# Kernel optimization log

Measured on AMD Instinct MI355X. Metric: run time of the kernel, lower is better.

Reference implementation:

```python
import jax, jax.numpy as jnp
import numpy as np

N = 50000      # node_size
D = 256        # node_F == rel_F (ent_F)
R = 1000       # rel_size
E = 300000     # triple_size == n_edges
DEPTH = 2
KSEL = E // 2  # rows rewritten by W_orth transform
NPROXY = 128


def l2n(x):
    # tf.nn.l2_normalize with eps=1e-12
    return x * jax.lax.rsqrt(jnp.maximum(jnp.sum(x * x, axis=-1, keepdims=True), 1e-12))


def setup_inputs() -> dict:
    key = jax.random.key(0)
    ks = jax.random.split(key, 12)
    features = jax.random.normal(ks[0], (N, D), jnp.float32)
    rel_emb = jax.random.normal(ks[1], (R, D), jnp.float32)
    p = jax.random.normal(ks[2], (N, 1), jnp.float32)            # dynamic_node_kernel
    w_keys = jax.random.normal(ks[3], (DEPTH, D, D), jnp.float32) / np.float32(np.sqrt(D))
    attn_kernels = jax.random.normal(ks[4], (DEPTH, D, 1), jnp.float32) * 0.1
    proxy = jax.random.normal(ks[5], (NPROXY, D * (DEPTH + 1)), jnp.float32) * 0.05
    gate_kernel = jax.random.normal(ks[6], (D * (DEPTH + 1), D * (DEPTH + 1)), jnp.float32) / np.float32(np.sqrt(D * (DEPTH + 1)))
    adj_row = jnp.sort(jax.random.randint(ks[7], (E,), 0, N))    # destination (segment) ids, sorted
    adj_col = jax.random.randint(ks[8], (E,), 0, N)              # neighbor ids
    rel_ids = jax.random.randint(ks[9], (E,), 0, R)              # relation id per triple/edge
    rel_vals = jax.random.uniform(ks[10], (E,), jnp.float32)     # sparse_val per triple
    new_indices = jax.random.randint(ks[11], (KSEL,), 0, E)      # rows updated by w_key
    return dict(features=features, rel_emb=rel_emb, p=p, w_keys=w_keys,
                attn_kernels=attn_kernels, proxy=proxy, gate_kernel=gate_kernel,
                rel_vals=rel_vals, adj_row=adj_row, adj_col=adj_col,
                rel_ids=rel_ids, new_indices=new_indices)


def reference(features, rel_emb, p, w_keys, attn_kernels, proxy, gate_kernel,
              rel_vals, adj_row, adj_col, rel_ids, new_indices):
    tanh_p = jnp.tanh(p)                                   # [N,1]
    feats = features * tanh_p                              # use_p scaling (activation=None -> identity)
    outputs = [feats]
    for l in range(DEPTH):
        # sparse (triple,rel) x rel_emb : one relation per triple -> gather + scale
        rels_sum = rel_vals[:, None] * rel_emb[rel_ids]    # [E,D]
        rels_sum = l2n(rels_sum)
        # W_orth: transform a subset of rows by w_key, scatter back
        src = rels_sum[new_indices] @ w_keys[l]            # [KSEL,D]
        rels_sum = rels_sum.at[new_indices].set(src)
        neighs = feats[adj_col]                            # [E,D] gather
        rels_sum = rels_sum * tanh_p[adj_col]              # use_p on neighbors
        # Householder-style reflection of neighbor features
        neighs = neighs - 2.0 * jnp.sum(neighs * rels_sum, axis=1, keepdims=True) * rels_sum
        # per-edge attention logits, softmax over incoming edges of each row node
        att = (rels_sum @ attn_kernels[l])[:, 0]           # [E]
        m = jax.ops.segment_max(att, adj_row, num_segments=N)      # [N]
        att = jnp.exp(att - m[adj_row])
        s = jax.ops.segment_sum(att, adj_row, num_segments=N)      # [N]
        att = att / s[adj_row]
        # weighted scatter-aggregate
        feats = jax.ops.segment_sum(neighs * att[:, None], adj_row, num_segments=N)  # [N,D]
        feats = feats * tanh_p
        outputs.append(feats)
    out = jnp.concatenate(outputs, axis=-1)                # [N, D*(DEPTH+1)]
    proxy_att = jax.nn.softmax(l2n(out) @ l2n(proxy).T, axis=-1)   # [N,128]
    proxy_feature = out - proxy_att @ proxy
    gate = jax.nn.sigmoid(proxy_feature @ gate_kernel)
    out = gate * out + (1.0 - gate) * proxy_feature
    return (out, p)
```

## Files before the change

kernel.cpp:

```cpp
#include <hip/hip_runtime.h>
#include <math.h>

#define D 256
#define DCAT 768
#define NPX 128
#define QSTR 896
#define CSTR 136

typedef __attribute__((ext_vector_type(8))) short bf16x8;
typedef __attribute__((ext_vector_type(4))) float f32x4;

__device__ __forceinline__ short cvt_bf16(float f){
  union { float f; unsigned u; } v; v.f = f;
  unsigned r = v.u + 0x7FFF + ((v.u >> 16) & 1);
  return (short)(r >> 16);
}
__device__ __forceinline__ float bf2f(short s){
  union { float f; unsigned u; } v; v.u = ((unsigned)(unsigned short)s) << 16;
  return v.f;
}

__device__ __forceinline__ float waveSum(float v){
#pragma unroll
  for(int o=32;o>=1;o>>=1) v += __shfl_xor(v,o,64);
  return v;
}
__device__ __forceinline__ float waveMax(float v){
#pragma unroll
  for(int o=32;o>=1;o>>=1) v = fmaxf(v,__shfl_xor(v,o,64));
  return v;
}

__global__ void k_setup(const float* __restrict__ rel_emb, const float* __restrict__ attn,
                        const float* __restrict__ w_keys, const float* __restrict__ proxy,
                        const float* __restrict__ gatek, const float* __restrict__ p,
                        const float* __restrict__ features,
                        const int* __restrict__ adj_row, const int* __restrict__ new_idx,
                        float* __restrict__ ss_rel, float* __restrict__ att_n,
                        float* __restrict__ att_t, short* __restrict__ reb,
                        short* __restrict__ rwb, short* __restrict__ pn,
                        short* __restrict__ BG, short* __restrict__ Bt2,
                        float* __restrict__ tp, int* __restrict__ rs,
                        unsigned char* __restrict__ flag, float* __restrict__ pout,
                        short* __restrict__ Q, float* __restrict__ ssn,
                        int R_, int n, int e, int ksel, int nprep){
  __shared__ float tile[32][33];
  __shared__ float tile2[32][33];
  __shared__ float sm[4];
  const int b = blockIdx.x, tid = threadIdx.x;
  const int lane = tid & 63, wv = tid >> 6;
  const int B2 = 3*R_+128, B3 = B2+576, B4 = B3+96, B5 = B4+96;
  const int B6 = B5+nprep;

  if(b < R_){
    int r = b, d = tid;
    float v = rel_emb[(size_t)r*D+d];
    reb[(size_t)r*D+d] = cvt_bf16(v);
    float s = waveSum(v*v);
    if(lane==0) sm[wv]=s;
    __syncthreads();
    if(tid==0) ss_rel[r]=sm[0]+sm[1]+sm[2]+sm[3];
    __syncthreads();
    for(int l=0;l<2;l++){
      float dd = waveSum(v*attn[l*D+d]);
      if(lane==0) sm[wv]=dd;
      __syncthreads();
      if(tid==0) att_n[(size_t)l*R_+r]=sm[0]+sm[1]+sm[2]+sm[3];
      __syncthreads();
    }
  } else if(b < 3*R_){
    int l = (b-R_) / R_, r = (b-R_) % R_, d = tid;
    const float* W = w_keys + (size_t)l*D*D;
    const float* ak = attn + (size_t)l*D;
    const float* row = rel_emb + (size_t)r*D;
    float acc=0.f;
#pragma unroll 4
    for(int k=0;k<D;k++) acc = fmaf(row[k], W[(size_t)k*D+d], acc);
    rwb[(size_t)l*R_*D + (size_t)r*D + d]=cvt_bf16(acc);
    float dd = waveSum(acc*ak[d]);
    if(lane==0) sm[wv]=dd;
    __syncthreads();
    if(tid==0) att_t[(size_t)l*R_+r]=sm[0]+sm[1]+sm[2]+sm[3];
  } else if(b < B2){
    int j = b - 3*R_;
    float v0 = proxy[(size_t)j*DCAT + tid];
    float v1 = proxy[(size_t)j*DCAT + 256 + tid];
    float v2 = proxy[(size_t)j*DCAT + 512 + tid];
    float ssum = waveSum(v0*v0 + v1*v1 + v2*v2);
    if(lane==0) sm[wv]=ssum;
    __syncthreads();
    float scale = rsqrtf(fmaxf(sm[0]+sm[1]+sm[2]+sm[3],1e-12f));
    pn[(size_t)j*DCAT + tid]       = cvt_bf16(v0*scale);
    pn[(size_t)j*DCAT + 256 + tid] = cvt_bf16(v1*scale);
    pn[(size_t)j*DCAT + 512 + tid] = cvt_bf16(v2*scale);
  } else if(b < B4){
    const float* in; short* out; int R, C, ldo, t;
    if(b < B3){ t = b-B2; in=gatek; out=BG;  R=DCAT; C=DCAT; ldo=QSTR; }
    else      { t = b-B3; in=proxy; out=Bt2; R=NPX;  C=DCAT; ldo=NPX;  }
    int bx = (t%24)*32, by = (t/24)*32;
    int tx = tid & 31, ty = tid >> 5;
    for(int i=ty;i<32;i+=8){
      int rr = by+i, cc = bx+tx;
      if(rr<R && cc<C) tile[i][tx] = in[(size_t)rr*C + cc];
    }
    __syncthreads();
    for(int i=ty;i<32;i+=8){
      int cc = bx+i, rr = by+tx;
      if(cc<C && rr<R) out[(size_t)cc*ldo + rr] = cvt_bf16(tile[tx][i]);
    }
  } else if(b < B5){
    int t = b - B4;
    int it = t / 24, jt = t % 24;
    int i0 = it*32, j0 = jt*32;
    int tx = tid & 31, ty = tid >> 5;
    float acc4[4] = {0.f,0.f,0.f,0.f};
    for(int k0=0;k0<DCAT;k0+=32){
      for(int rr=ty;rr<32;rr+=8){
        tile[rr][tx]  = proxy[(size_t)(i0+rr)*DCAT + k0+tx];
        tile2[rr][tx] = gatek[(size_t)(k0+rr)*DCAT + j0+tx];
      }
      __syncthreads();
#pragma unroll 8
      for(int kk=0;kk<32;kk++){
        float bv = tile2[kk][tx];
        acc4[0] = fmaf(tile[ty][kk],    bv, acc4[0]);
        acc4[1] = fmaf(tile[ty+8][kk],  bv, acc4[1]);
        acc4[2] = fmaf(tile[ty+16][kk], bv, acc4[2]);
        acc4[3] = fmaf(tile[ty+24][kk], bv, acc4[3]);
      }
      __syncthreads();
    }
#pragma unroll
    for(int k=0;k<4;k++)
      BG[(size_t)(j0+tx)*QSTR + DCAT + i0 + ty + 8*k] = cvt_bf16(-acc4[k]);
  } else if(b < B6){
    int t = b - B5;
    int i = t*256 + tid;
    if(i<n){ float pv = p[i]; tp[i]=tanhf(pv); pout[i]=pv; }
    if(i<=n){
      int lo=0, hi=e;
      while(lo<hi){ int mid=(lo+hi)>>1; if(adj_row[mid]<i) lo=mid+1; else hi=mid; }
      rs[i]=lo;
    }
    if(i<ksel) flag[new_idx[i]] = 1;
  } else {
    int row = b - B6;
    if(row < n){
      float t0 = tanhf(p[row]);
      float v = features[(size_t)row*D + tid] * t0;
      Q[(size_t)row*QSTR + tid] = cvt_bf16(v);
      float s = waveSum(v*v);
      if(lane==0) sm[wv]=s;
      __syncthreads();
      if(tid==0) ssn[row] = sm[0]+sm[1]+sm[2]+sm[3];
    }
  }
}

__global__ void k_agg(const int* __restrict__ rs, const int* __restrict__ adj_col,
                      const int* __restrict__ rel_ids, const float* __restrict__ rel_vals,
                      const unsigned char* __restrict__ flag, const float* __restrict__ tp,
                      const float* __restrict__ ss_rel, const float* __restrict__ att_n,
                      const float* __restrict__ att_t, const short* __restrict__ reb,
                      const short* __restrict__ rwb, short* __restrict__ Q,
                      float* __restrict__ ssn, int n, int layer){
  int wid = threadIdx.x>>6, lane = threadIdx.x&63;
  int node = blockIdx.x*4 + wid;
  if(node>=n) return;
  int s = rs[node], e = rs[node+1];
  float accq[16];
#pragma unroll
  for(int k=0;k<16;k++) accq[k]=0.f;

  auto logit = [&](int i)->float{
    int rid = rel_ids[i]; float rv = rel_vals[i];
    float a = 0.f;
    if(rv>0.f){
      float t = tp[adj_col[i]];
      float sc = rv*rsqrtf(fmaxf(rv*rv*ss_rel[rid],1e-12f));
      a = t*sc*(flag[i]? att_t[rid] : att_n[rid]);
    }
    return a;
  };

  if(e > s){
    float aF = 0.f, mxl = -INFINITY;
    {
      int i = s + lane;
      if(i < e){
        aF = logit(i);
        mxl = aF;
        for(i += 64; i < e; i += 64) mxl = fmaxf(mxl, logit(i));
      }
    }
    float mx = waveMax(mxl);
    float sel = (s+lane < e) ? __expf(aF - mx) : 0.f;
    for(int i = s+64+lane; i < e; i += 64) sel += __expf(logit(i) - mx);
    float se = waveSum(sel);
    float inv = 1.f/se;

    int qid = lane>>4, ql = lane&15;
    int j0 = s + qid;
    bool valid = j0 < e;
    int col=0, rid=0; float rv=0.f; bool fl=false;
    bf16x8 pn0={}, pn1={}, pr0={}, pr1={};
    if(valid){
      col=adj_col[j0]; rid=rel_ids[j0]; rv=rel_vals[j0]; fl=flag[j0];
      const short* np = Q + (size_t)col*QSTR + layer*D + ql*16;
      pn0 = *(const bf16x8*)np; pn1 = *(const bf16x8*)(np+8);
      if(rv>0.f){
        const short* rp = (fl? rwb : reb) + (size_t)rid*D + ql*16;
        pr0 = *(const bf16x8*)rp; pr1 = *(const bf16x8*)(rp+8);
      }
    }
    for(int i0=s; i0<e; i0+=4){
      int jn = i0 + 4 + qid;
      bool vn = jn < e;
      int coln=0, ridn=0; float rvn=0.f; bool fln=false;
      bf16x8 qn0={}, qn1={}, qr0={}, qr1={};
      if(vn){
        coln=adj_col[jn]; ridn=rel_ids[jn]; rvn=rel_vals[jn]; fln=flag[jn];
        const short* np = Q + (size_t)coln*QSTR + layer*D + ql*16;
        qn0 = *(const bf16x8*)np; qn1 = *(const bf16x8*)(np+8);
        if(rvn>0.f){
          const short* rp = (fln? rwb : reb) + (size_t)ridn*D + ql*16;
          qr0 = *(const bf16x8*)rp; qr1 = *(const bf16x8*)(rp+8);
        }
      }
      float w=0.f, coef=0.f;
      float nbv[16], rbv[16];
#pragma unroll
      for(int k=0;k<8;k++){
        nbv[k]=bf2f(pn0[k]); nbv[k+8]=bf2f(pn1[k]);
        rbv[k]=bf2f(pr0[k]); rbv[k+8]=bf2f(pr1[k]);
      }
      if(valid){
        if(rv>0.f){
          float t = tp[col];
          float sc = rv*rsqrtf(fmaxf(rv*rv*ss_rel[rid],1e-12f));
          float dp = 0.f;
#pragma unroll
          for(int k=0;k<16;k++) dp += nbv[k]*rbv[k];
#pragma unroll
          for(int o=1;o<16;o<<=1) dp += __shfl_xor(dp,o,64);
          float a = t*sc*(fl? att_t[rid] : att_n[rid]);
          w = __expf(a-mx)*inv;
          coef = 2.f*t*t*sc*sc*dp;
        } else {
          w = __expf(-mx)*inv;
        }
      }
#pragma unroll
      for(int k=0;k<16;k++) accq[k] += w*(nbv[k] - coef*rbv[k]);

      valid=vn; col=coln; rid=ridn; rv=rvn; fl=fln;
      pn0=qn0; pn1=qn1; pr0=qr0; pr1=qr1;
    }
  }
#pragma unroll
  for(int k=0;k<16;k++){
    float v = accq[k];
    v += __shfl_xor(v,16,64);
    v += __shfl_xor(v,32,64);
    accq[k] = v;
  }
  if(lane < 16){
    float t0 = tp[node];
    bf16x8 o0, o1;
    float pss = 0.f;
#pragma unroll
    for(int k=0;k<8;k++){
      o0[k]=cvt_bf16(accq[k]*t0); o1[k]=cvt_bf16(accq[k+8]*t0);
      pss += accq[k]*accq[k] + accq[k+8]*accq[k+8];
    }
    short* op = Q + (size_t)node*QSTR + (layer+1)*D + lane*16;
    *(bf16x8*)op = o0;
    *(bf16x8*)(op+8) = o1;
#pragma unroll
    for(int o=1;o<16;o<<=1) pss += __shfl_xor(pss,o,64);
    if(lane==0) ssn[node] += pss * t0 * t0;
  }
}

__global__ __launch_bounds__(256,2) void k_pr(
    short* __restrict__ Q, const short* __restrict__ pn,
    const float* __restrict__ ssn, int M)
{
  __shared__ short smem[3][2][128*32];
  const int tid = threadIdx.x, lane = tid & 63, w = tid >> 6;
  const int wm = w >> 1, wn = w & 1;
  int nwg = gridDim.y;
  int orig = blockIdx.y;
  int q = nwg>>3, rm = nwg&7, xcd = orig&7, lid = orig>>3;
  int wg = (xcd<rm ? xcd*(q+1) : rm*(q+1)+(xcd-rm)*q) + lid;
  const int bm = wg*128;

  const short* Ag = Q + (size_t)bm * QSTR;
  const short* Bg = pn;

  auto stage = [&](int buf, int k0){
#pragma unroll
    for(int c=0;c<2;++c){
      int u = c*256 + tid;
      int row = u >> 2;
      int cb = ((u & 3) ^ ((u >> 3) & 3)) * 8;
      __builtin_amdgcn_global_load_lds(
        (const __attribute__((address_space(1))) unsigned int*)(Ag + (size_t)row*QSTR + k0 + cb),
        (__attribute__((address_space(3))) unsigned int*)&smem[buf][0][u*8], 16, 0, 0);
      __builtin_amdgcn_global_load_lds(
        (const __attribute__((address_space(1))) unsigned int*)(Bg + (size_t)row*DCAT + k0 + cb),
        (__attribute__((address_space(3))) unsigned int*)&smem[buf][1][u*8], 16, 0, 0);
    }
  };

  f32x4 acc[4][4] = {};
  const int lr = lane & 15, kg = lane >> 4;
  const int ksw = (kg ^ ((lr >> 1) & 3)) * 8;
  constexpr int NT = DCAT / 32;

  stage(0, 0);
  stage(1, 32);
  for(int t=0; t<NT; ++t){
    if(t+1 < NT) asm volatile("s_waitcnt vmcnt(4)" ::: "memory");
    else         asm volatile("s_waitcnt vmcnt(0)" ::: "memory");
    __builtin_amdgcn_s_barrier();
    __builtin_amdgcn_sched_barrier(0);
    const short* Al = &smem[t%3][0][0];
    const short* Bl = &smem[t%3][1][0];
    bf16x8 af[4], bfr[4];
#pragma unroll
    for(int i=0;i<4;++i) af[i] = *(const bf16x8*)(Al + (wm*64 + i*16 + lr)*32 + ksw);
#pragma unroll
    for(int j=0;j<4;++j) bfr[j] = *(const bf16x8*)(Bl + (wn*64 + j*16 + lr)*32 + ksw);
    if(t+2 < NT) stage((t+2)%3, (t+2)*32);
    __builtin_amdgcn_s_setprio(1);
#pragma unroll
    for(int i=0;i<4;++i)
#pragma unroll
      for(int j=0;j<4;++j)
        acc[i][j] = __builtin_amdgcn_mfma_f32_16x16x32_bf16(af[i], bfr[j], acc[i][j], 0, 0, 0);
    __builtin_amdgcn_s_setprio(0);
  }

  __syncthreads();
  short* lg = (short*)smem;
  const int row0l = wm*64 + kg*4;
  const int col0l = wn*64 + lr;
#pragma unroll
  for(int i=0;i<4;++i){
#pragma unroll
    for(int j=0;j<4;++j){
#pragma unroll
      for(int r=0;r<4;++r){
        int rl = row0l + i*16 + r;
        int rg = bm + rl;
        float s = (rg < M) ? rsqrtf(fmaxf(ssn[rg],1e-12f)) : 0.f;
        lg[rl*132 + col0l + j*16] = cvt_bf16(acc[i][j][r] * s);
      }
    }
  }
  __syncthreads();
  for(int k2=0;k2<32;++k2){
    int rl = w*32 + k2;
    float a = bf2f(lg[rl*132 + lane]);
    float b = bf2f(lg[rl*132 + 64 + lane]);
    float m = waveMax(fmaxf(a,b));
    float ea = __expf(a-m), eb = __expf(b-m);
    float sm_ = waveSum(ea+eb);
    float inv = 1.f/sm_;
    size_t rg = (size_t)(bm + rl);
    Q[rg*QSTR + DCAT + lane]      = cvt_bf16(ea*inv);
    Q[rg*QSTR + DCAT + 64 + lane] = cvt_bf16(eb*inv);
  }
}

__global__ __launch_bounds__(256,2) void k_go(
    short* __restrict__ Q, const short* __restrict__ BG,
    const short* __restrict__ Bt2, float* __restrict__ outF, int M)
{
  __shared__ short smem[3][2][128*32];
  const int tid = threadIdx.x, lane = tid & 63, w = tid >> 6;
  const int wm = w >> 1, wn = w & 1;
  const int gx = gridDim.x;
  int nwg = gx*gridDim.y;
  int orig = blockIdx.y*gx + blockIdx.x;
  int q = nwg>>3, rm = nwg&7, xcd = orig&7, lid = orig>>3;
  int wg = (xcd<rm ? xcd*(q+1) : rm*(q+1)+(xcd-rm)*q) + lid;
  const int bn = (wg%gx)*128, bm = (wg/gx)*128;
  const int lr = lane & 15, kg = lane >> 4;

  const short* Ag = Q  + (size_t)bm * QSTR;
  const short* Bg = BG + (size_t)bn * QSTR;

  auto stage = [&](int buf, int k0){
#pragma unroll
    for(int c=0;c<2;++c){
      int u = c*256 + tid;
      int row = u >> 2;
      int cb = ((u & 3) ^ ((u >> 3) & 3)) * 8;
      __builtin_amdgcn_global_load_lds(
        (const __attribute__((address_space(1))) unsigned int*)(Ag + (size_t)row*QSTR + k0 + cb),
        (__attribute__((address_space(3))) unsigned int*)&smem[buf][0][u*8], 16, 0, 0);
      __builtin_amdgcn_global_load_lds(
        (const __attribute__((address_space(1))) unsigned int*)(Bg + (size_t)row*QSTR + k0 + cb),
        (__attribute__((address_space(3))) unsigned int*)&smem[buf][1][u*8], 16, 0, 0);
    }
  };

  stage(0, 0);
  stage(1, 32);

  f32x4 acc[4][4] = {};
#pragma unroll
  for(int ks=0; ks<4; ++ks){
    bf16x8 af[4], bb[4];
#pragma unroll
    for(int i=0;i<4;++i)
      af[i] = *(const bf16x8*)(Q + (size_t)(bm + wm*64 + i*16 + lr)*QSTR + DCAT + ks*32 + kg*8);
#pragma unroll
    for(int j=0;j<4;++j)
      bb[j] = *(const bf16x8*)(Bt2 + (size_t)(bn + wn*64 + j*16 + lr)*NPX + ks*32 + kg*8);
#pragma unroll
    for(int i=0;i<4;++i)
#pragma unroll
      for(int j=0;j<4;++j)
        acc[i][j] = __builtin_amdgcn_mfma_f32_16x16x32_bf16(af[i], bb[j], acc[i][j], 0, 0, 0);
  }
  short4 pvb[4][4];
#pragma unroll
  for(int i=0;i<4;++i)
#pragma unroll
    for(int j=0;j<4;++j){
      pvb[i][j].x = cvt_bf16(acc[i][j][0]);
      pvb[i][j].y = cvt_bf16(acc[i][j][1]);
      pvb[i][j].z = cvt_bf16(acc[i][j][2]);
      pvb[i][j].w = cvt_bf16(acc[i][j][3]);
      acc[i][j] = (f32x4){0.f,0.f,0.f,0.f};
    }

  const int ksw = (kg ^ ((lr >> 1) & 3)) * 8;
  constexpr int NT = QSTR / 32;
  for(int t=0; t<NT; ++t){
    if(t+1 < NT) asm volatile("s_waitcnt vmcnt(4)" ::: "memory");
    else         asm volatile("s_waitcnt vmcnt(0)" ::: "memory");
    __builtin_amdgcn_s_barrier();
    __builtin_amdgcn_sched_barrier(0);
    const short* Al = &smem[t%3][0][0];
    const short* Bl = &smem[t%3][1][0];
    bf16x8 af[4], bfr[4];
#pragma unroll
    for(int i=0;i<4;++i) af[i] = *(const bf16x8*)(Al + (wm*64 + i*16 + lr)*32 + ksw);
#pragma unroll
    for(int j=0;j<4;++j) bfr[j] = *(const bf16x8*)(Bl + (wn*64 + j*16 + lr)*32 + ksw);
    if(t+2 < NT) stage((t+2)%3, (t+2)*32);
    __builtin_amdgcn_s_setprio(1);
#pragma unroll
    for(int i=0;i<4;++i)
#pragma unroll
      for(int j=0;j<4;++j)
        acc[i][j] = __builtin_amdgcn_mfma_f32_16x16x32_bf16(af[i], bfr[j], acc[i][j], 0, 0, 0);
    __builtin_amdgcn_s_setprio(0);
  }

  __syncthreads();
  short* cst = (short*)smem;
  const int row0l = wm*64 + kg*4;
  const int col0l = wn*64 + lr;
#pragma unroll
  for(int i=0;i<4;++i){
#pragma unroll
    for(int j=0;j<4;++j){
      float pv4[4] = { bf2f(pvb[i][j].x), bf2f(pvb[i][j].y), bf2f(pvb[i][j].z), bf2f(pvb[i][j].w) };
#pragma unroll
      for(int r2=0;r2<4;++r2){
        float g = 1.f/(1.f+__expf(-acc[i][j][r2]));
        cst[(row0l + i*16 + r2)*CSTR + col0l + j*16] = cvt_bf16((1.f-g)*pv4[r2]);
      }
    }
  }
  __syncthreads();
  const int rl0 = tid>>4, c0 = (tid&15)*8;
#pragma unroll
  for(int rr=0; rr<8; ++rr){
    int rl = rl0 + rr*16;
    int rg = bm + rl;
    if(rg >= M) continue;
    bf16x8 c8  = *(const bf16x8*)(cst + rl*CSTR + c0);
    bf16x8 oc8 = *(const bf16x8*)(Q + (size_t)rg*QSTR + bn + c0);
    float ov[8];
#pragma unroll
    for(int k=0;k<8;k++) ov[k] = bf2f(oc8[k]) - bf2f(c8[k]);
    *(float4*)(outF + (size_t)rg*DCAT + bn + c0)     = make_float4(ov[0],ov[1],ov[2],ov[3]);
    *(float4*)(outF + (size_t)rg*DCAT + bn + c0 + 4) = make_float4(ov[4],ov[5],ov[6],ov[7]);
  }
}

extern "C" void kernel_launch(void* const* d_in, const int* in_sizes, int n_in,
                              void* d_out, int out_size, void* d_ws, size_t ws_size,
                              hipStream_t stream){
  const float* features = (const float*)d_in[0];
  const float* rel_emb  = (const float*)d_in[1];
  const float* p        = (const float*)d_in[2];
  const float* w_keys   = (const float*)d_in[3];
  const float* attn     = (const float*)d_in[4];
  const float* proxy    = (const float*)d_in[5];
  const float* gatek    = (const float*)d_in[6];
  const float* rel_vals = (const float*)d_in[7];
  const int* adj_row    = (const int*)d_in[8];
  const int* adj_col    = (const int*)d_in[9];
  const int* rel_ids    = (const int*)d_in[10];
  const int* new_idx    = (const int*)d_in[11];

  const int n    = in_sizes[2];
  const int r    = in_sizes[1]/D;
  const int e    = in_sizes[7];
  const int ksel = in_sizes[11];
  const size_t Mpad = ((size_t)n + 127) & ~(size_t)127;

  char* ws = (char*)d_ws;
  size_t off=0;
  auto alloc=[&](size_t bytes)->void*{ void* pp = ws+off; off=(off+bytes+255)&~(size_t)255; return pp; };
  float* tp      = (float*)alloc((size_t)n*4);
  int*   rs      = (int*)alloc((size_t)(n+1)*4);
  unsigned char* flag = (unsigned char*)alloc((size_t)e);
  float* ss_rel  = (float*)alloc((size_t)r*4);
  float* att_n   = (float*)alloc((size_t)2*r*4);
  float* att_t   = (float*)alloc((size_t)2*r*4);
  short* reb     = (short*)alloc((size_t)r*D*2);
  short* rwb     = (short*)alloc((size_t)2*r*D*2);
  short* pn      = (short*)alloc((size_t)NPX*DCAT*2);
  short* Bt2     = (short*)alloc((size_t)DCAT*NPX*2);
  short* BG      = (short*)alloc((size_t)DCAT*QSTR*2);
  float* ssn     = (float*)alloc(Mpad*4);
  short* Q       = (short*)alloc(Mpad*QSTR*2);

  float* outF = (float*)d_out;
  float* pout = (float*)d_out + (size_t)n*DCAT;

  hipMemsetAsync(flag, 0, (size_t)e, stream);
  hipMemsetAsync(Q + (size_t)n*QSTR, 0, (Mpad-(size_t)n)*QSTR*2, stream);

  {
    int prep_n = (ksel > n+1 ? ksel : n+1);
    int nprep = (prep_n+255)/256;
    int nblocks = 3*r + 128 + 576 + 96 + 96 + nprep + n;
    k_setup<<<nblocks,256,0,stream>>>(rel_emb, attn, w_keys, proxy, gatek, p, features,
                                      adj_row, new_idx,
                                      ss_rel, att_n, att_t, reb, rwb, pn,
                                      BG, Bt2, tp, rs, flag, pout, Q, ssn,
                                      r, n, e, ksel, nprep);
  }

  for(int l=0;l<2;l++)
    k_agg<<<(n+3)/4,256,0,stream>>>(rs,adj_col,rel_ids,rel_vals,flag,tp,ss_rel,
                                    att_n+(size_t)l*r, att_t+(size_t)l*r, reb,
                                    rwb+(size_t)l*r*D, Q, ssn, n, l);

  int mt = (int)(Mpad/128);
  k_pr<<<dim3(1, mt),256,0,stream>>>(Q, pn, ssn, n);
  k_go<<<dim3(DCAT/128, mt),256,0,stream>>>(Q, BG, Bt2, outF, n);
}
```

Baseline: 436.8 us.

## Fuse proxy-attention softmax kernel into gate/output GEMM kernel

Merges the proxy-logit GEMM and softmax kernel into the gate/output kernel. Each block now computes proxy logits alongside the gate GEMM over the 768-wide K, and keeps the softmaxed attention in LDS for the two 128-K GEMMs. This removes one launch and the write and re-read of the proxy attention through global memory. In exchange, each of the six column tiles recomputes the same proxy logits, roughly doubling MFMA work in the main loop and raising LDS use per block.

```diff
diff --git a/kernel.cpp b/kernel.cpp
--- a/kernel.cpp
+++ b/kernel.cpp
@@ -5,6 +5,7 @@
 #define DCAT 768
 #define NPX 128
 #define QSTR 896
+#define LSTR 136
 #define CSTR 136
 
 typedef __attribute__((ext_vector_type(8))) short bf16x8;
@@ -282,103 +283,12 @@
   }
 }
 
-__global__ __launch_bounds__(256,2) void k_pr(
-    short* __restrict__ Q, const short* __restrict__ pn,
-    const float* __restrict__ ssn, int M)
+__global__ __launch_bounds__(256,2) void k_tail(
+    const short* __restrict__ Q, const short* __restrict__ BG,
+    const short* __restrict__ Bt2, const short* __restrict__ pn,
+    const float* __restrict__ ssn, float* __restrict__ outF, int M)
 {
-  __shared__ short smem[3][2][128*32];
-  const int tid = threadIdx.x, lane = tid & 63, w = tid >> 6;
-  const int wm = w >> 1, wn = w & 1;
-  int nwg = gridDim.y;
-  int orig = blockIdx.y;
-  int q = nwg>>3, rm = nwg&7, xcd = orig&7, lid = orig>>3;
-  int wg = (xcd<rm ? xcd*(q+1) : rm*(q+1)+(xcd-rm)*q) + lid;
-  const int bm = wg*128;
-
-  const short* Ag = Q + (size_t)bm * QSTR;
-  const short* Bg = pn;
-
-  auto stage = [&](int buf, int k0){
-#pragma unroll
-    for(int c=0;c<2;++c){
-      int u = c*256 + tid;
-      int row = u >> 2;
-      int cb = ((u & 3) ^ ((u >> 3) & 3)) * 8;
-      __builtin_amdgcn_global_load_lds(
-        (const __attribute__((address_space(1))) unsigned int*)(Ag + (size_t)row*QSTR + k0 + cb),
-        (__attribute__((address_space(3))) unsigned int*)&smem[buf][0][u*8], 16, 0, 0);
-      __builtin_amdgcn_global_load_lds(
-        (const __attribute__((address_space(1))) unsigned int*)(Bg + (size_t)row*DCAT + k0 + cb),
-        (__attribute__((address_space(3))) unsigned int*)&smem[buf][1][u*8], 16, 0, 0);
-    }
-  };
-
-  f32x4 acc[4][4] = {};
-  const int lr = lane & 15, kg = lane >> 4;
-  const int ksw = (kg ^ ((lr >> 1) & 3)) * 8;
-  constexpr int NT = DCAT / 32;
-
-  stage(0, 0);
-  stage(1, 32);
-  for(int t=0; t<NT; ++t){
-    if(t+1 < NT) asm volatile("s_waitcnt vmcnt(4)" ::: "memory");
-    else         asm volatile("s_waitcnt vmcnt(0)" ::: "memory");
-    __builtin_amdgcn_s_barrier();
-    __builtin_amdgcn_sched_barrier(0);
-    const short* Al = &smem[t%3][0][0];
-    const short* Bl = &smem[t%3][1][0];
-    bf16x8 af[4], bfr[4];
-#pragma unroll
-    for(int i=0;i<4;++i) af[i] = *(const bf16x8*)(Al + (wm*64 + i*16 + lr)*32 + ksw);
-#pragma unroll
-    for(int j=0;j<4;++j) bfr[j] = *(const bf16x8*)(Bl + (wn*64 + j*16 + lr)*32 + ksw);
-    if(t+2 < NT) stage((t+2)%3, (t+2)*32);
-    __builtin_amdgcn_s_setprio(1);
-#pragma unroll
-    for(int i=0;i<4;++i)
-#pragma unroll
-      for(int j=0;j<4;++j)
-        acc[i][j] = __builtin_amdgcn_mfma_f32_16x16x32_bf16(af[i], bfr[j], acc[i][j], 0, 0, 0);
-    __builtin_amdgcn_s_setprio(0);
-  }
-
-  __syncthreads();
-  short* lg = (short*)smem;
-  const int row0l = wm*64 + kg*4;
-  const int col0l = wn*64 + lr;
-#pragma unroll
-  for(int i=0;i<4;++i){
-#pragma unroll
-    for(int j=0;j<4;++j){
-#pragma unroll
-      for(int r=0;r<4;++r){
-        int rl = row0l + i*16 + r;
-        int rg = bm + rl;
-        float s = (rg < M) ? rsqrtf(fmaxf(ssn[rg],1e-12f)) : 0.f;
-        lg[rl*132 + col0l + j*16] = cvt_bf16(acc[i][j][r] * s);
-      }
-    }
-  }
-  __syncthreads();
-  for(int k2=0;k2<32;++k2){
-    int rl = w*32 + k2;
-    float a = bf2f(lg[rl*132 + lane]);
-    float b = bf2f(lg[rl*132 + 64 + lane]);
-    float m = waveMax(fmaxf(a,b));
-    float ea = __expf(a-m), eb = __expf(b-m);
-    float sm_ = waveSum(ea+eb);
-    float inv = 1.f/sm_;
-    size_t rg = (size_t)(bm + rl);
-    Q[rg*QSTR + DCAT + lane]      = cvt_bf16(ea*inv);
-    Q[rg*QSTR + DCAT + 64 + lane] = cvt_bf16(eb*inv);
-  }
-}
-
-__global__ __launch_bounds__(256,2) void k_go(
-    short* __restrict__ Q, const short* __restrict__ BG,
-    const short* __restrict__ Bt2, float* __restrict__ outF, int M)
-{
-  __shared__ short smem[3][2][128*32];
+  __shared__ short smem[3][3][128*32];
   const int tid = threadIdx.x, lane = tid & 63, w = tid >> 6;
   const int wm = w >> 1, wn = w & 1;
   const int gx = gridDim.x;
@@ -404,6 +314,9 @@
       __builtin_amdgcn_global_load_lds(
         (const __attribute__((address_space(1))) unsigned int*)(Bg + (size_t)row*QSTR + k0 + cb),
         (__attribute__((address_space(3))) unsigned int*)&smem[buf][1][u*8], 16, 0, 0);
+      __builtin_amdgcn_global_load_lds(
+        (const __attribute__((address_space(1))) unsigned int*)(pn + (size_t)row*DCAT + k0 + cb),
+        (__attribute__((address_space(3))) unsigned int*)&smem[buf][2][u*8], 16, 0, 0);
     }
   };
 
@@ -411,47 +324,24 @@
   stage(1, 32);
 
   f32x4 acc[4][4] = {};
-#pragma unroll
-  for(int ks=0; ks<4; ++ks){
-    bf16x8 af[4], bb[4];
-#pragma unroll
-    for(int i=0;i<4;++i)
-      af[i] = *(const bf16x8*)(Q + (size_t)(bm + wm*64 + i*16 + lr)*QSTR + DCAT + ks*32 + kg*8);
-#pragma unroll
-    for(int j=0;j<4;++j)
-      bb[j] = *(const bf16x8*)(Bt2 + (size_t)(bn + wn*64 + j*16 + lr)*NPX + ks*32 + kg*8);
-#pragma unroll
-    for(int i=0;i<4;++i)
-#pragma unroll
-      for(int j=0;j<4;++j)
-        acc[i][j] = __builtin_amdgcn_mfma_f32_16x16x32_bf16(af[i], bb[j], acc[i][j], 0, 0, 0);
-  }
-  short4 pvb[4][4];
-#pragma unroll
-  for(int i=0;i<4;++i)
-#pragma unroll
-    for(int j=0;j<4;++j){
-      pvb[i][j].x = cvt_bf16(acc[i][j][0]);
-      pvb[i][j].y = cvt_bf16(acc[i][j][1]);
-      pvb[i][j].z = cvt_bf16(acc[i][j][2]);
-      pvb[i][j].w = cvt_bf16(acc[i][j][3]);
-      acc[i][j] = (f32x4){0.f,0.f,0.f,0.f};
-    }
-
+  f32x4 acc2[4][4] = {};
   const int ksw = (kg ^ ((lr >> 1) & 3)) * 8;
-  constexpr int NT = QSTR / 32;
+  constexpr int NT = DCAT / 32;
   for(int t=0; t<NT; ++t){
-    if(t+1 < NT) asm volatile("s_waitcnt vmcnt(4)" ::: "memory");
+    if(t+1 < NT) asm volatile("s_waitcnt vmcnt(6)" ::: "memory");
     else         asm volatile("s_waitcnt vmcnt(0)" ::: "memory");
     __builtin_amdgcn_s_barrier();
     __builtin_amdgcn_sched_barrier(0);
     const short* Al = &smem[t%3][0][0];
     const short* Bl = &smem[t%3][1][0];
-    bf16x8 af[4], bfr[4];
-#pragma unroll
-    for(int i=0;i<4;++i) af[i] = *(const bf16x8*)(Al + (wm*64 + i*16 + lr)*32 + ksw);
+    const short* Pl = &smem[t%3][2][0];
+    bf16x8 af[4], bfr[4], pfr[4];
+#pragma unroll
+    for(int i=0;i<4;++i) af[i]  = *(const bf16x8*)(Al + (wm*64 + i*16 + lr)*32 + ksw);
 #pragma unroll
     for(int j=0;j<4;++j) bfr[j] = *(const bf16x8*)(Bl + (wn*64 + j*16 + lr)*32 + ksw);
+#pragma unroll
+    for(int j=0;j<4;++j) pfr[j] = *(const bf16x8*)(Pl + (wn*64 + j*16 + lr)*32 + ksw);
     if(t+2 < NT) stage((t+2)%3, (t+2)*32);
     __builtin_amdgcn_s_setprio(1);
 #pragma unroll
@@ -459,22 +349,88 @@
 #pragma unroll
       for(int j=0;j<4;++j)
         acc[i][j] = __builtin_amdgcn_mfma_f32_16x16x32_bf16(af[i], bfr[j], acc[i][j], 0, 0, 0);
+#pragma unroll
+    for(int i=0;i<4;++i)
+#pragma unroll
+      for(int j=0;j<4;++j)
+        acc2[i][j] = __builtin_amdgcn_mfma_f32_16x16x32_bf16(af[i], pfr[j], acc2[i][j], 0, 0, 0);
     __builtin_amdgcn_s_setprio(0);
   }
 
   __syncthreads();
-  short* cst = (short*)smem;
+  short* lg = (short*)smem;
   const int row0l = wm*64 + kg*4;
   const int col0l = wn*64 + lr;
 #pragma unroll
   for(int i=0;i<4;++i){
 #pragma unroll
     for(int j=0;j<4;++j){
-      float pv4[4] = { bf2f(pvb[i][j].x), bf2f(pvb[i][j].y), bf2f(pvb[i][j].z), bf2f(pvb[i][j].w) };
+#pragma unroll
+      for(int r=0;r<4;++r){
+        int rl = row0l + i*16 + r;
+        int rg = bm + rl;
+        float s = (rg < M) ? rsqrtf(fmaxf(ssn[rg],1e-12f)) : 0.f;
+        lg[rl*LSTR + col0l + j*16] = cvt_bf16(acc2[i][j][r] * s);
+      }
+    }
+  }
+  __syncthreads();
+  for(int k2=0;k2<32;++k2){
+    int rl = w*32 + k2;
+    float a = bf2f(lg[rl*LSTR + lane]);
+    float b = bf2f(lg[rl*LSTR + 64 + lane]);
+    float m = waveMax(fmaxf(a,b));
+    float ea = __expf(a-m), eb = __expf(b-m);
+    float sm_ = waveSum(ea+eb);
+    float inv = 1.f/sm_;
+    lg[rl*LSTR + lane]      = cvt_bf16(ea*inv);
+    lg[rl*LSTR + 64 + lane] = cvt_bf16(eb*inv);
+  }
+  __syncthreads();
+
+#pragma unroll
+  for(int ks=0; ks<4; ++ks){
+    bf16x8 af2[4], bb[4];
+#pragma unroll
+    for(int i=0;i<4;++i)
+      af2[i] = *(const bf16x8*)(lg + (wm*64 + i*16 + lr)*LSTR + ks*32 + kg*8);
+#pragma unroll
+    for(int j=0;j<4;++j)
+      bb[j] = *(const bf16x8*)(BG + (size_t)(bn + wn*64 + j*16 + lr)*QSTR + DCAT + ks*32 + kg*8);
+#pragma unroll
+    for(int i=0;i<4;++i)
+#pragma unroll
+      for(int j=0;j<4;++j)
+        acc[i][j] = __builtin_amdgcn_mfma_f32_16x16x32_bf16(af2[i], bb[j], acc[i][j], 0, 0, 0);
+  }
+
+  f32x4 pvacc[4][4] = {};
+#pragma unroll
+  for(int ks=0; ks<4; ++ks){
+    bf16x8 af2[4], bb[4];
+#pragma unroll
+    for(int i=0;i<4;++i)
+      af2[i] = *(const bf16x8*)(lg + (wm*64 + i*16 + lr)*LSTR + ks*32 + kg*8);
+#pragma unroll
+    for(int j=0;j<4;++j)
+      bb[j] = *(const bf16x8*)(Bt2 + (size_t)(bn + wn*64 + j*16 + lr)*NPX + ks*32 + kg*8);
+#pragma unroll
+    for(int i=0;i<4;++i)
+#pragma unroll
+      for(int j=0;j<4;++j)
+        pvacc[i][j] = __builtin_amdgcn_mfma_f32_16x16x32_bf16(af2[i], bb[j], pvacc[i][j], 0, 0, 0);
+  }
+
+  short* cst = (short*)smem + 128*LSTR;
+#pragma unroll
+  for(int i=0;i<4;++i){
+#pragma unroll
+    for(int j=0;j<4;++j){
 #pragma unroll
       for(int r2=0;r2<4;++r2){
+        float pv4 = bf2f(cvt_bf16(pvacc[i][j][r2]));
         float g = 1.f/(1.f+__expf(-acc[i][j][r2]));
-        cst[(row0l + i*16 + r2)*CSTR + col0l + j*16] = cvt_bf16((1.f-g)*pv4[r2]);
+        cst[(row0l + i*16 + r2)*CSTR + col0l + j*16] = cvt_bf16((1.f-g)*pv4);
       }
     }
   }
@@ -557,6 +513,5 @@
                                     rwb+(size_t)l*r*D, Q, ssn, n, l);
 
   int mt = (int)(Mpad/128);
-  k_pr<<<dim3(1, mt),256,0,stream>>>(Q, pn, ssn, n);
-  k_go<<<dim3(DCAT/128, mt),256,0,stream>>>(Q, BG, Bt2, outF, n);
-}
+  k_tail<<<dim3(DCAT/128, mt),256,0,stream>>>(Q, BG, Bt2, pn, ssn, outF, n);
+}
```

Result: slower. 527.3 us (+20.7%).
